# Kernel optimization log

Hardware: AMD Instinct MI355X
Metric: run time of the kernel (lower is better)

## Reference

```python
import jax, jax.numpy as jnp
import numpy as np

N, M, D = 16384, 4096, 512
TEMP = 1.0


def setup_inputs() -> dict:
    key = jax.random.key(0)
    kx, ky = jax.random.split(key)
    x = jax.random.normal(kx, (N, D), dtype=jnp.float32)
    y = jax.random.normal(ky, (M, D), dtype=jnp.float32)
    return {"x": x, "y": y, "temperature": 1}


def reference(x, y, temperature):
    # euclidean_distances_logits:
    #   logits = -0.5 * T * sum_d (x[n,None,:] - y[None,m,:])**2
    # Fused form avoiding the O(n*m*d) broadcast intermediate (same math):
    t = jnp.asarray(temperature, dtype=x.dtype) * jnp.float32(TEMP)
    x_sq = jnp.sum(x * x, axis=1, keepdims=True)          # [n, 1]
    y_sq = jnp.sum(y * y, axis=1)[None, :]                # [1, m]
    xy = jnp.einsum("nd,md->nm", x, y)                    # [n, m]
    sq_dist = x_sq - 2.0 * xy + y_sq                      # [n, m]
    return -0.5 * t * sq_dist
```

## Files before the change

### kernel.cpp

```cpp
#include <hip/hip_runtime.h>
#include <hip/hip_bf16.h>


#define NN 16384
#define MM 4096
#define DD 512

using frag_ab = __attribute__((ext_vector_type(8))) short;
using floatx4 = __attribute__((ext_vector_type(4))) float;

using gas_ptr = const __attribute__((address_space(1))) void*;
using las_ptr = __attribute__((address_space(3))) void*;

__device__ __forceinline__ void async_copy16(const void* g, void* l) {
    __builtin_amdgcn_global_load_lds((gas_ptr)g, (las_ptr)l, 16, 0, 0);
}

__device__ __forceinline__ unsigned bf16rne(float f) {
    union { float f; unsigned u; } v; v.f = f;
    unsigned u = v.u + 0x7FFFu + ((v.u >> 16) & 1u);
    return u >> 16;
}

__device__ __forceinline__ uint2 cvt4(float4 v) {
    uint2 r;
    r.x = bf16rne(v.x) | (bf16rne(v.y) << 16);
    r.y = bf16rne(v.z) | (bf16rne(v.w) << 16);
    return r;
}

__global__ void prep_kernel(const float* __restrict__ v, float* __restrict__ sq,
                            unsigned short* __restrict__ vb) {
    const int lane = threadIdx.x & 63;
    const int row  = blockIdx.x * 4 + (threadIdx.x >> 6);
    const float* p = v + (size_t)row * DD + lane * 8;
    float4 a = *(const float4*)(p);
    float4 b = *(const float4*)(p + 4);
    uint2 lo = cvt4(a), hi = cvt4(b);
    *(uint4*)(vb + (size_t)row * DD + lane * 8) = make_uint4(lo.x, lo.y, hi.x, hi.y);
    float s = a.x*a.x + a.y*a.y + a.z*a.z + a.w*a.w
            + b.x*b.x + b.y*b.y + b.z*b.z + b.w*b.w;
    #pragma unroll
    for (int off = 32; off > 0; off >>= 1) s += __shfl_xor(s, off);
    if (lane == 0) sq[row] = s;
}

__global__ void rowsq_kernel(const float* __restrict__ v, float* __restrict__ sq) {
    const int lane = threadIdx.x & 63;
    const int row  = blockIdx.x * 4 + (threadIdx.x >> 6);
    const float* p = v + (size_t)row * DD + lane * 8;
    float4 a = *(const float4*)(p);
    float4 b = *(const float4*)(p + 4);
    float s = a.x*a.x + a.y*a.y + a.z*a.z + a.w*a.w
            + b.x*b.x + b.y*b.y + b.z*b.z + b.w*b.w;
    #pragma unroll
    for (int off = 32; off > 0; off >>= 1) s += __shfl_xor(s, off);
    if (lane == 0) sq[row] = s;
}

__global__ __launch_bounds__(256) void protonet_gemm_bf(
    const unsigned short* __restrict__ xb, const unsigned short* __restrict__ yb,
    const float* __restrict__ xsq, const float* __restrict__ ysq,
    const int* __restrict__ temp, float* __restrict__ out)
{
    __shared__ __align__(16) unsigned short As[128 * 32];
    __shared__ __align__(16) unsigned short Bs[128 * 32];

    const int bn   = blockIdx.x;
    const int bm   = blockIdx.y;
    const int tid  = threadIdx.x;
    const int lane = tid & 63;
    const int wave = tid >> 6;
    const int wn   = wave & 1;
    const int wm   = wave >> 1;
    const int l15  = lane & 15;
    const int quad = lane >> 4;

    floatx4 acc[4][4] = {};

    const unsigned short* ga0 = xb + (size_t)(bn * 128 + (wave * 2 + 0) * 16 + l15) * DD + quad * 8;
    const unsigned short* ga1 = xb + (size_t)(bn * 128 + (wave * 2 + 1) * 16 + l15) * DD + quad * 8;
    const unsigned short* gb0 = yb + (size_t)(bm * 128 + (wave * 2 + 0) * 16 + l15) * DD + quad * 8;
    const unsigned short* gb1 = yb + (size_t)(bm * 128 + (wave * 2 + 1) * 16 + l15) * DD + quad * 8;

    for (int k0 = 0; k0 < DD; k0 += 32) {
        async_copy16(ga0 + k0, As + (wave * 2 + 0) * 512);
        async_copy16(ga1 + k0, As + (wave * 2 + 1) * 512);
        async_copy16(gb0 + k0, Bs + (wave * 2 + 0) * 512);
        async_copy16(gb1 + k0, Bs + (wave * 2 + 1) * 512);
        __syncthreads();

        frag_ab a[4], b[4];
        #pragma unroll
        for (int t = 0; t < 4; ++t) {
            a[t] = *(const frag_ab*)(As + (wn * 4 + t) * 512 + lane * 8);
            b[t] = *(const frag_ab*)(Bs + (wm * 4 + t) * 512 + lane * 8);
        }
        #pragma unroll
        for (int tn = 0; tn < 4; ++tn)
            #pragma unroll
            for (int tm = 0; tm < 4; ++tm)
                acc[tn][tm] = __builtin_amdgcn_mfma_f32_16x16x32_bf16(
                    a[tn], b[tm], acc[tn][tm], 0, 0, 0);
        __syncthreads();
    }

    const float t = (float)(*temp);
    const int n_base = bn * 128 + wn * 64;
    const int m_base = bm * 128 + wm * 64;
    #pragma unroll
    for (int tn = 0; tn < 4; ++tn) {
        float xs[4];
        #pragma unroll
        for (int r = 0; r < 4; ++r) xs[r] = xsq[n_base + tn * 16 + quad * 4 + r];
        #pragma unroll
        for (int tm = 0; tm < 4; ++tm) {
            const int mcol = m_base + tm * 16 + l15;
            const float ys = ysq[mcol];
            #pragma unroll
            for (int r = 0; r < 4; ++r) {
                const int nrow = n_base + tn * 16 + quad * 4 + r;
                out[(size_t)nrow * MM + mcol] = t * (acc[tn][tm][r] - 0.5f * (xs[r] + ys));
            }
        }
    }
}

__global__ __launch_bounds__(256) void protonet_gemm(
    const float* __restrict__ x, const float* __restrict__ y,
    const float* __restrict__ xsq, const float* __restrict__ ysq,
    const int* __restrict__ temp, float* __restrict__ out)
{
    __shared__ __align__(16) unsigned short As[128 * 32];
    __shared__ __align__(16) unsigned short Bs[128 * 32];

    const int bn   = blockIdx.x;
    const int bm   = blockIdx.y;
    const int tid  = threadIdx.x;
    const int lane = tid & 63;
    const int wave = tid >> 6;
    const int wn   = wave & 1;
    const int wm   = wave >> 1;
    const int l15  = lane & 15;
    const int quad = lane >> 4;

    floatx4 acc[4][4] = {};

    for (int k0 = 0; k0 < DD; k0 += 32) {
        #pragma unroll
        for (int i = 0; i < 4; ++i) {
            int c = tid + i * 256;
            int row = c >> 3, col4 = c & 7;
            float4 v = *(const float4*)(x + (size_t)(bn * 128 + row) * DD + k0 + col4 * 4);
            *(uint2*)(&As[row * 32 + col4 * 4]) = cvt4(v);
        }
        #pragma unroll
        for (int i = 0; i < 4; ++i) {
            int c = tid + i * 256;
            int row = c >> 3, col4 = c & 7;
            float4 v = *(const float4*)(y + (size_t)(bm * 128 + row) * DD + k0 + col4 * 4);
            *(uint2*)(&Bs[row * 32 + col4 * 4]) = cvt4(v);
        }
        __syncthreads();

        frag_ab a[4], b[4];
        #pragma unroll
        for (int t = 0; t < 4; ++t) {
            a[t] = *(const frag_ab*)(&As[(wn * 64 + t * 16 + l15) * 32 + quad * 8]);
            b[t] = *(const frag_ab*)(&Bs[(wm * 64 + t * 16 + l15) * 32 + quad * 8]);
        }
        #pragma unroll
        for (int tn = 0; tn < 4; ++tn)
            #pragma unroll
            for (int tm = 0; tm < 4; ++tm)
                acc[tn][tm] = __builtin_amdgcn_mfma_f32_16x16x32_bf16(
                    a[tn], b[tm], acc[tn][tm], 0, 0, 0);
        __syncthreads();
    }

    const float t = (float)(*temp);
    const int n_base = bn * 128 + wn * 64;
    const int m_base = bm * 128 + wm * 64;
    #pragma unroll
    for (int tn = 0; tn < 4; ++tn) {
        float xs[4];
        #pragma unroll
        for (int r = 0; r < 4; ++r) xs[r] = xsq[n_base + tn * 16 + quad * 4 + r];
        #pragma unroll
        for (int tm = 0; tm < 4; ++tm) {
            const int mcol = m_base + tm * 16 + l15;
            const float ys = ysq[mcol];
            #pragma unroll
            for (int r = 0; r < 4; ++r) {
                const int nrow = n_base + tn * 16 + quad * 4 + r;
                out[(size_t)nrow * MM + mcol] = t * (acc[tn][tm][r] - 0.5f * (xs[r] + ys));
            }
        }
    }
}

extern "C" void kernel_launch(void* const* d_in, const int* in_sizes, int n_in,
                              void* d_out, int out_size, void* d_ws, size_t ws_size,
                              hipStream_t stream) {
    const float* x    = (const float*)d_in[0];
    const float* y    = (const float*)d_in[1];
    const int*   temp = (const int*)d_in[2];
    float* out = (float*)d_out;

    float* xsq = (float*)d_ws;
    float* ysq = xsq + NN;
    unsigned short* xb = (unsigned short*)(ysq + MM);
    unsigned short* yb = xb + (size_t)NN * DD;

    const size_t need = (size_t)(NN + MM) * 4 + (size_t)(NN + MM) * DD * 2;

    if (ws_size >= need) {
        prep_kernel<<<NN / 4, 256, 0, stream>>>(x, xsq, xb);
        prep_kernel<<<MM / 4, 256, 0, stream>>>(y, ysq, yb);
        protonet_gemm_bf<<<dim3(NN / 128, MM / 128), 256, 0, stream>>>(
            xb, yb, xsq, ysq, temp, out);
    } else {
        rowsq_kernel<<<NN / 4, 256, 0, stream>>>(x, xsq);
        rowsq_kernel<<<MM / 4, 256, 0, stream>>>(y, ysq);
        protonet_gemm<<<dim3(NN / 128, MM / 128), 256, 0, stream>>>(
            x, y, xsq, ysq, temp, out);
    }
}
```

Before: 419.5 us.

## Load MFMA fragments directly from global into registers with double buffering

Replaces the LDS-staged bf16 GEMM with a version where each wave loads its A/B fragments straight from global memory into registers. Loads for the next k-step are double-buffered while the current one runs on the MFMAs, and there are no barriers. The grid is transposed so consecutive blocks share the same x row tile, and the x-norm load is vectorized. The trade-off is that LDS reuse is gone, so each wave fetches its fragments separately (twice the global/L2 traffic per block), and register pressure rises.

Result: slower. 513.1 us (+22.3%).

```diff
diff --git a/kernel.cpp b/kernel.cpp
--- a/kernel.cpp
+++ b/kernel.cpp
@@ -8,13 +8,6 @@
 
 using frag_ab = __attribute__((ext_vector_type(8))) short;
 using floatx4 = __attribute__((ext_vector_type(4))) float;
-
-using gas_ptr = const __attribute__((address_space(1))) void*;
-using las_ptr = __attribute__((address_space(3))) void*;
-
-__device__ __forceinline__ void async_copy16(const void* g, void* l) {
-    __builtin_amdgcn_global_load_lds((gas_ptr)g, (las_ptr)l, 16, 0, 0);
-}
 
 __device__ __forceinline__ unsigned bf16rne(float f) {
     union { float f; unsigned u; } v; v.f = f;
@@ -58,8 +51,74 @@
     if (lane == 0) sq[row] = s;
 }
 
-__global__ __launch_bounds__(256) void protonet_gemm_bf(
+__global__ __launch_bounds__(256) void protonet_gemm_reg(
     const unsigned short* __restrict__ xb, const unsigned short* __restrict__ yb,
+    const float* __restrict__ xsq, const float* __restrict__ ysq,
+    const int* __restrict__ temp, float* __restrict__ out)
+{
+    const int bm   = blockIdx.x;
+    const int bn   = blockIdx.y;
+    const int tid  = threadIdx.x;
+    const int lane = tid & 63;
+    const int wave = tid >> 6;
+    const int wn   = wave & 1;
+    const int wm   = wave >> 1;
+    const int l15  = lane & 15;
+    const int quad = lane >> 4;
+
+    floatx4 acc[4][4] = {};
+
+    const unsigned short* abase = xb + (size_t)(bn * 128 + wn * 64 + l15) * DD + quad * 8;
+    const unsigned short* bbase = yb + (size_t)(bm * 128 + wm * 64 + l15) * DD + quad * 8;
+
+    frag_ab a[2][4], b[2][4];
+    #pragma unroll
+    for (int t = 0; t < 4; ++t) {
+        a[0][t] = *(const frag_ab*)(abase + (size_t)t * 16 * DD);
+        b[0][t] = *(const frag_ab*)(bbase + (size_t)t * 16 * DD);
+    }
+
+    int s = 0;
+    #pragma unroll
+    for (int k0 = 0; k0 < DD; k0 += 32) {
+        if (k0 + 32 < DD) {
+            #pragma unroll
+            for (int t = 0; t < 4; ++t) {
+                a[s ^ 1][t] = *(const frag_ab*)(abase + (size_t)t * 16 * DD + k0 + 32);
+                b[s ^ 1][t] = *(const frag_ab*)(bbase + (size_t)t * 16 * DD + k0 + 32);
+            }
+        }
+        #pragma unroll
+        for (int tn = 0; tn < 4; ++tn)
+            #pragma unroll
+            for (int tm = 0; tm < 4; ++tm)
+                acc[tn][tm] = __builtin_amdgcn_mfma_f32_16x16x32_bf16(
+                    a[s][tn], b[s][tm], acc[s == 0 ? tn : tn][tm], 0, 0, 0);
+        s ^= 1;
+    }
+
+    const float t = (float)(*temp);
+    const int n_base = bn * 128 + wn * 64;
+    const int m_base = bm * 128 + wm * 64;
+    #pragma unroll
+    for (int tn = 0; tn < 4; ++tn) {
+        float4 xs = *(const float4*)(xsq + n_base + tn * 16 + quad * 4);
+        #pragma unroll
+        for (int tm = 0; tm < 4; ++tm) {
+            const int mcol = m_base + tm * 16 + l15;
+            const float ys = ysq[mcol];
+            const float* xsp = (const float*)&xs;
+            #pragma unroll
+            for (int r = 0; r < 4; ++r) {
+                const int nrow = n_base + tn * 16 + quad * 4 + r;
+                out[(size_t)nrow * MM + mcol] = t * (acc[tn][tm][r] - 0.5f * (xsp[r] + ys));
+            }
+        }
+    }
+}
+
+__global__ __launch_bounds__(256) void protonet_gemm(
+    const float* __restrict__ x, const float* __restrict__ y,
     const float* __restrict__ xsq, const float* __restrict__ ysq,
     const int* __restrict__ temp, float* __restrict__ out)
 {
@@ -78,74 +137,6 @@
 
     floatx4 acc[4][4] = {};
 
-    const unsigned short* ga0 = xb + (size_t)(bn * 128 + (wave * 2 + 0) * 16 + l15) * DD + quad * 8;
-    const unsigned short* ga1 = xb + (size_t)(bn * 128 + (wave * 2 + 1) * 16 + l15) * DD + quad * 8;
-    const unsigned short* gb0 = yb + (size_t)(bm * 128 + (wave * 2 + 0) * 16 + l15) * DD + quad * 8;
-    const unsigned short* gb1 = yb + (size_t)(bm * 128 + (wave * 2 + 1) * 16 + l15) * DD + quad * 8;
-
-    for (int k0 = 0; k0 < DD; k0 += 32) {
-        async_copy16(ga0 + k0, As + (wave * 2 + 0) * 512);
-        async_copy16(ga1 + k0, As + (wave * 2 + 1) * 512);
-        async_copy16(gb0 + k0, Bs + (wave * 2 + 0) * 512);
-        async_copy16(gb1 + k0, Bs + (wave * 2 + 1) * 512);
-        __syncthreads();
-
-        frag_ab a[4], b[4];
-        #pragma unroll
-        for (int t = 0; t < 4; ++t) {
-            a[t] = *(const frag_ab*)(As + (wn * 4 + t) * 512 + lane * 8);
-            b[t] = *(const frag_ab*)(Bs + (wm * 4 + t) * 512 + lane * 8);
-        }
-        #pragma unroll
-        for (int tn = 0; tn < 4; ++tn)
-            #pragma unroll
-            for (int tm = 0; tm < 4; ++tm)
-                acc[tn][tm] = __builtin_amdgcn_mfma_f32_16x16x32_bf16(
-                    a[tn], b[tm], acc[tn][tm], 0, 0, 0);
-        __syncthreads();
-    }
-
-    const float t = (float)(*temp);
-    const int n_base = bn * 128 + wn * 64;
-    const int m_base = bm * 128 + wm * 64;
-    #pragma unroll
-    for (int tn = 0; tn < 4; ++tn) {
-        float xs[4];
-        #pragma unroll
-        for (int r = 0; r < 4; ++r) xs[r] = xsq[n_base + tn * 16 + quad * 4 + r];
-        #pragma unroll
-        for (int tm = 0; tm < 4; ++tm) {
-            const int mcol = m_base + tm * 16 + l15;
-            const float ys = ysq[mcol];
-            #pragma unroll
-            for (int r = 0; r < 4; ++r) {
-                const int nrow = n_base + tn * 16 + quad * 4 + r;
-                out[(size_t)nrow * MM + mcol] = t * (acc[tn][tm][r] - 0.5f * (xs[r] + ys));
-            }
-        }
-    }
-}
-
-__global__ __launch_bounds__(256) void protonet_gemm(
-    const float* __restrict__ x, const float* __restrict__ y,
-    const float* __restrict__ xsq, const float* __restrict__ ysq,
-    const int* __restrict__ temp, float* __restrict__ out)
-{
-    __shared__ __align__(16) unsigned short As[128 * 32];
-    __shared__ __align__(16) unsigned short Bs[128 * 32];
-
-    const int bn   = blockIdx.x;
-    const int bm   = blockIdx.y;
-    const int tid  = threadIdx.x;
-    const int lane = tid & 63;
-    const int wave = tid >> 6;
-    const int wn   = wave & 1;
-    const int wm   = wave >> 1;
-    const int l15  = lane & 15;
-    const int quad = lane >> 4;
-
-    floatx4 acc[4][4] = {};
-
     for (int k0 = 0; k0 < DD; k0 += 32) {
         #pragma unroll
         for (int i = 0; i < 4; ++i) {
@@ -217,7 +208,7 @@
     if (ws_size >= need) {
         prep_kernel<<<NN / 4, 256, 0, stream>>>(x, xsq, xb);
         prep_kernel<<<MM / 4, 256, 0, stream>>>(y, ysq, yb);
-        protonet_gemm_bf<<<dim3(NN / 128, MM / 128), 256, 0, stream>>>(
+        protonet_gemm_reg<<<dim3(MM / 128, NN / 128), 256, 0, stream>>>(
             xb, yb, xsq, ysq, temp, out);
     } else {
         rowsq_kernel<<<NN / 4, 256, 0, stream>>>(x, xsq);
```
